# Kernel optimization log

Hardware: AMD Instinct MI355X
Metric: run time of the kernel (lower is better)

## Reference

```python
import jax, jax.numpy as jnp
import numpy as np

N = 100000
E = 3200000
IN_F = 256
OUT_F = 256


def setup_inputs() -> dict:
    key = jax.random.key(0)
    k1, k2, k3, k4, k5 = jax.random.split(key, 5)
    stdv = 1.0 / np.sqrt(OUT_F)
    x = jax.random.normal(k1, (N, IN_F), dtype=jnp.float32)
    edge_index = jax.random.randint(k2, (2, E), 0, N, dtype=jnp.int64)
    edge_weight = jax.random.uniform(k3, (E,), dtype=jnp.float32)
    weight = jax.random.uniform(k4, (IN_F, OUT_F), dtype=jnp.float32, minval=-stdv, maxval=stdv)
    bias = jax.random.uniform(k5, (OUT_F,), dtype=jnp.float32, minval=-stdv, maxval=stdv)
    return {"x": x, "edge_index": edge_index, "edge_weight": edge_weight,
            "weight": weight, "bias": bias}


def reference(x, edge_index, edge_weight, weight, bias):
    # Dense transform: [N, in] @ [in, out] -> [N, out]
    support = x @ weight
    row, col = edge_index[0], edge_index[1]
    # SpMM: out[row] += edge_weight * support[col]
    messages = edge_weight[:, None] * support[col]  # [E, out]
    output = jax.ops.segment_sum(messages, row, num_segments=N)  # [N, out]
    return output + bias
```

## Files before the change

kernel.cpp:

```cpp
#include <hip/hip_runtime.h>
#include <hip/hip_fp16.h>

#define IN_F 256
#define OUT_F 256
#define HALF_F 128
#define RPB_SHIFT 9
#define RPB (1 << RPB_SHIFT)
#define NBINS_MAX 256
#define TILE_E 4096
#define XS_PAD 40
#define SHARD_SHIFT 14

using bf16x8 = __attribute__((ext_vector_type(8))) short;
using bf16x4 = __attribute__((ext_vector_type(4))) short;
using f32x4  = __attribute__((ext_vector_type(4))) float;
using ull    = unsigned long long;

__device__ inline short bf16rne(float f) {
    unsigned u = __float_as_uint(f);
    u = u + 0x7FFFu + ((u >> 16) & 1u);
    return (short)(u >> 16);
}
__device__ inline unsigned pack_half2(float a, float b) {
    __half2 h = __floats2half2_rn(a, b);
    return *reinterpret_cast<unsigned*>(&h);
}

__global__ __launch_bounds__(256) void convert_wt_kernel(
    const float* __restrict__ w, short* __restrict__ wt)
{
    const int idx = blockIdx.x * blockDim.x + threadIdx.x;
    const int c = idx >> 8, k = idx & 255;
    wt[(size_t)c * IN_F + k] = bf16rne(w[(size_t)k * OUT_F + c]);
}

__global__ __launch_bounds__(256) void mfma_gemm_kernel(
    const float* __restrict__ x, const short* __restrict__ wt,
    __half* __restrict__ supA, __half* __restrict__ supB, int M)
{
    __shared__ short xs[2][32][XS_PAD];

    const int t    = threadIdx.x;
    const int lane = t & 63;
    const int wid  = t >> 6;
    const int l15  = lane & 15;
    const int l4   = lane >> 4;
    const int rowbase = blockIdx.x * 32;
    const int cbase   = wid * 64;

    const int srow = t >> 3;
    const int sks  = (t & 7) * 4;
    int grow = rowbase + srow; if (grow > M - 1) grow = M - 1;
    const float* xsrc = x + (size_t)grow * IN_F + sks;

    f32x4 acc[2][4];
#pragma unroll
    for (int rt = 0; rt < 2; ++rt)
#pragma unroll
        for (int ct = 0; ct < 4; ++ct)
            acc[rt][ct] = (f32x4){0.f, 0.f, 0.f, 0.f};

    const short* wp[4];
#pragma unroll
    for (int ct = 0; ct < 4; ++ct)
        wp[ct] = wt + (size_t)(cbase + ct * 16 + l15) * IN_F + l4 * 8;

    {
        const float4 f = *(const float4*)xsrc;
        bf16x4 v;
        v[0] = bf16rne(f.x); v[1] = bf16rne(f.y);
        v[2] = bf16rne(f.z); v[3] = bf16rne(f.w);
        *(bf16x4*)&xs[0][srow][sks] = v;
    }
    __syncthreads();

#pragma unroll
    for (int k0 = 0; k0 < 8; ++k0) {
        const int cur = k0 & 1;

        float4 nf;
        if (k0 < 7) nf = *(const float4*)(xsrc + (k0 + 1) * 32);

        bf16x8 b[4];
#pragma unroll
        for (int ct = 0; ct < 4; ++ct)
            b[ct] = *(const bf16x8*)(wp[ct] + k0 * 32);

        bf16x8 a[2];
#pragma unroll
        for (int rt = 0; rt < 2; ++rt)
            a[rt] = *(const bf16x8*)&xs[cur][rt * 16 + l15][l4 * 8];

#pragma unroll
        for (int rt = 0; rt < 2; ++rt)
#pragma unroll
            for (int ct = 0; ct < 4; ++ct)
                acc[rt][ct] = __builtin_amdgcn_mfma_f32_16x16x32_bf16(
                    b[ct], a[rt], acc[rt][ct], 0, 0, 0);

        if (k0 < 7) {
            bf16x4 v;
            v[0] = bf16rne(nf.x); v[1] = bf16rne(nf.y);
            v[2] = bf16rne(nf.z); v[3] = bf16rne(nf.w);
            *(bf16x4*)&xs[cur ^ 1][srow][sks] = v;
        }
        __syncthreads();
    }

    __half* dst = (wid < 2) ? supA : supB;
    const int fbase = (wid & 1) * 64;
#pragma unroll
    for (int rt = 0; rt < 2; ++rt) {
        const int r = rowbase + rt * 16 + l15;
        if (r >= M) continue;
#pragma unroll
        for (int ct = 0; ct < 4; ++ct) {
            uint2 pk;
            pk.x = pack_half2(acc[rt][ct][0], acc[rt][ct][1]);
            pk.y = pack_half2(acc[rt][ct][2], acc[rt][ct][3]);
            *(uint2*)(dst + (size_t)r * HALF_F + fbase + ct * 16 + l4 * 4) = pk;
        }
    }
}

__global__ __launch_bounds__(256) void a1a_hist_kernel(
    const int* __restrict__ ei, int* __restrict__ thist, int E)
{
    __shared__ int hist[NBINS_MAX];
    const int tid = threadIdx.x;
    hist[tid] = 0;
    __syncthreads();
    const int base = blockIdx.x * TILE_E;
#pragma unroll
    for (int i = 0; i < TILE_E / 256; ++i) {
        const int e = base + i * 256 + tid;
        if (e < E)
            atomicAdd(&hist[__builtin_nontemporal_load(ei + e) >> RPB_SHIFT], 1);
    }
    __syncthreads();
    thist[(size_t)blockIdx.x * NBINS_MAX + tid] = hist[tid];
}

__global__ __launch_bounds__(256) void tile_scan_kernel(
    int* __restrict__ thist, int* __restrict__ btot, int T)
{
    const int b   = blockIdx.x;
    const int tid = threadIdx.x;
    __shared__ int s[256];
    int carry = 0;
    for (int c0 = 0; c0 < T; c0 += 256) {
        const int t = c0 + tid;
        const int v = (t < T) ? thist[(size_t)t * NBINS_MAX + b] : 0;
        s[tid] = v;
        __syncthreads();
        for (int d = 1; d < 256; d <<= 1) {
            const int u = (tid >= d) ? s[tid - d] : 0;
            __syncthreads();
            s[tid] += u;
            __syncthreads();
        }
        const int total = s[255];
        if (t < T) thist[(size_t)t * NBINS_MAX + b] = carry + s[tid] - v;
        carry += total;
        __syncthreads();
    }
    if (tid == 0) btot[b] = carry;
}

__global__ __launch_bounds__(NBINS_MAX) void bin_scan_kernel(
    const int* __restrict__ btot, int* __restrict__ bstart, int nbins)
{
    __shared__ int s[NBINS_MAX];
    const int tid = threadIdx.x;
    const int v = (tid < nbins) ? btot[tid] : 0;
    s[tid] = v;
    __syncthreads();
    for (int d = 1; d < NBINS_MAX; d <<= 1) {
        const int u = (tid >= d) ? s[tid - d] : 0;
        __syncthreads();
        s[tid] += u;
        __syncthreads();
    }
    bstart[tid] = s[tid] - v;
}

__global__ __launch_bounds__(256) void a1b_scatter_kernel(
    const int* __restrict__ ei, const float* __restrict__ ew,
    const int* __restrict__ bstart, const int* __restrict__ thist,
    ull* __restrict__ tscw, int E)
{
    __shared__ int hist[NBINS_MAX];
    __shared__ int rbase[NBINS_MAX];
    const int tid = threadIdx.x;
    hist[tid]  = 0;
    rbase[tid] = bstart[tid] + thist[(size_t)blockIdx.x * NBINS_MAX + tid];
    __syncthreads();
    const int base = blockIdx.x * TILE_E;
#pragma unroll
    for (int i = 0; i < TILE_E / 256; ++i) {
        const int e = base + i * 256 + tid;
        if (e < E) {
            const int      row = __builtin_nontemporal_load(ei + e);
            const int      col = __builtin_nontemporal_load(ei + E + e);
            const unsigned wb  = __builtin_nontemporal_load((const unsigned*)ew + e);
            const int b   = row >> RPB_SHIFT;
            const int rnk = atomicAdd(&hist[b], 1);
            tscw[rbase[b] + rnk] = ((ull)wb << 32) |
                                   ((unsigned)col << RPB_SHIFT) |
                                   (unsigned)(row & (RPB - 1));
        }
    }
}

__global__ __launch_bounds__(256) void a2_sort_kernel(
    const ull* __restrict__ tscw, const int* __restrict__ bstart,
    const int* __restrict__ btot, int* __restrict__ counts,
    int* __restrict__ cursor, ull* __restrict__ scw, int M)
{
    const int b   = blockIdx.x;
    const int tid = threadIdx.x;
    const int n   = btot[b];
    const int s0  = bstart[b];

    __shared__ int hcur[RPB * 8];
    __shared__ int hbase[RPB * 8];
    __shared__ int s[256];

#pragma unroll
    for (int k = 0; k < 16; ++k) hcur[tid + k * 256] = 0;
    __syncthreads();

    for (int i = tid; i < n; i += 256) {
        const ull en = __builtin_nontemporal_load(tscw + s0 + i);
        const int key = ((int)(en & (RPB - 1)) << 3) |
                        (int)((en >> (RPB_SHIFT + SHARD_SHIFT)) & 7u);
        atomicAdd(&hcur[key], 1);
    }
    __syncthreads();

    int loc[16];
    int run = 0;
#pragma unroll
    for (int k = 0; k < 16; ++k) { loc[k] = hcur[tid * 16 + k]; run += loc[k]; }
    s[tid] = run;
    __syncthreads();
    for (int d = 1; d < 256; d <<= 1) {
        const int u = (tid >= d) ? s[tid - d] : 0;
        __syncthreads();
        s[tid] += u;
        __syncthreads();
    }
    int accum = s[tid] - run;
#pragma unroll
    for (int k = 0; k < 16; ++k) { hbase[tid * 16 + k] = accum; accum += loc[k]; }
    __syncthreads();

    {
        const int r0 = 2 * tid, r1 = r0 + 1;
        const int st0  = hbase[r0 << 3];
        const int st1  = hbase[r1 << 3];
        const int end1 = (r1 == RPB - 1) ? n : hbase[(r1 + 1) << 3];
        const int gr0 = (b << RPB_SHIFT) + r0, gr1 = gr0 + 1;
        if (gr0 < M) { counts[gr0] = st1 - st0;  cursor[gr0] = s0 + st0; }
        if (gr1 < M) { counts[gr1] = end1 - st1; cursor[gr1] = s0 + st1; }
    }
#pragma unroll
    for (int k = 0; k < 16; ++k) hcur[tid * 16 + k] = s0 + hbase[tid * 16 + k];
    __syncthreads();

    for (int i = tid; i < n; i += 256) {
        const ull en = __builtin_nontemporal_load(tscw + s0 + i);
        const int key = ((int)(en & (RPB - 1)) << 3) |
                        (int)((en >> (RPB_SHIFT + SHARD_SHIFT)) & 7u);
        const int pos = atomicAdd(&hcur[key], 1);
        scw[pos] = (en & 0xFFFFFFFF00000000ull) |
                   (unsigned)((en >> RPB_SHIFT) & 0x1FFFFu);
    }
}

__global__ __launch_bounds__(256) void pull_half_kernel(
    const int* __restrict__ counts, const int* __restrict__ cursor,
    const ull* __restrict__ scw, const __half* __restrict__ suph,
    const float* __restrict__ biash, float* __restrict__ outh, int M)
{
    const int wv  = blockIdx.x * 4 + (threadIdx.x >> 6);
    const int row = wv * 2 + ((threadIdx.x >> 5) & 1);
    if (row >= M) return;
    const int l = threadIdx.x & 31;

    const int cnt   = counts[row];
    const int start = cursor[row];

    float4 acc = *(const float4*)(biash + l * 4);

#define GATHER_FMA_H(pe)                                                      \
    {                                                                         \
        const int   c  = (int)(unsigned)(pe);                                 \
        const float wj = __uint_as_float((unsigned)((pe) >> 32));             \
        const uint2 v = *(const uint2*)(suph + (size_t)c * HALF_F + l * 4);   \
        const float2 f0 = __half22float2(*(const __half2*)&v.x);              \
        const float2 f1 = __half22float2(*(const __half2*)&v.y);              \
        acc.x = fmaf(wj, f0.x, acc.x); acc.y = fmaf(wj, f0.y, acc.y);         \
        acc.z = fmaf(wj, f1.x, acc.z); acc.w = fmaf(wj, f1.y, acc.w);         \
    }

    for (int j0 = 0; j0 < cnt; j0 += 32) {
        ull pr = 0ull;
        if (j0 + l < cnt)
            pr = __builtin_nontemporal_load(scw + start + j0 + l);
        const int m = min(32, cnt - j0);

        int j = 0;
        for (; j + 4 <= m; j += 4) {
            const ull p0 = __shfl(pr, j, 32),     p1 = __shfl(pr, j + 1, 32);
            const ull p2 = __shfl(pr, j + 2, 32), p3 = __shfl(pr, j + 3, 32);
            GATHER_FMA_H(p0); GATHER_FMA_H(p1);
            GATHER_FMA_H(p2); GATHER_FMA_H(p3);
        }
        for (; j < m; ++j) {
            const ull p = __shfl(pr, j, 32);
            GATHER_FMA_H(p);
        }
    }
#undef GATHER_FMA_H

    f32x4 o; o[0] = acc.x; o[1] = acc.y; o[2] = acc.z; o[3] = acc.w;
    __builtin_nontemporal_store(o, (f32x4*)(outh + (size_t)row * OUT_F + l * 4));
}

__global__ __launch_bounds__(256) void bias_init_kernel(
    float* __restrict__ out, const float* __restrict__ bias, int total4)
{
    const float4* b4 = (const float4*)bias;
    float4* o4 = (float4*)out;
    for (int i = blockIdx.x * blockDim.x + threadIdx.x; i < total4;
         i += gridDim.x * blockDim.x)
        o4[i] = b4[i & 63];
}

__global__ __launch_bounds__(256) void edge_scatter_kernel(
    const int* __restrict__ ei, const float* __restrict__ ew,
    const __half* __restrict__ supA, const __half* __restrict__ supB,
    float* __restrict__ out, int E)
{
    const int e = blockIdx.x * 4 + (threadIdx.x >> 6);
    if (e >= E) return;
    const int lane = threadIdx.x & 63;
    const int   row = ei[e];
    const int   col = ei[E + e];
    const float wgt = ew[e];
    const __half* src = (lane < 32) ? supA : supB;
    const int fl = (lane & 31) * 4;
    const uint2 v = *(const uint2*)(src + (size_t)col * HALF_F + fl);
    const float2 f0 = __half22float2(*(const __half2*)&v.x);
    const float2 f1 = __half22float2(*(const __half2*)&v.y);
    float* o = out + (size_t)row * OUT_F + (lane >> 5) * HALF_F + fl;
    unsafeAtomicAdd(o + 0, wgt * f0.x);
    unsafeAtomicAdd(o + 1, wgt * f0.y);
    unsafeAtomicAdd(o + 2, wgt * f1.x);
    unsafeAtomicAdd(o + 3, wgt * f1.y);
}

extern "C" void kernel_launch(void* const* d_in, const int* in_sizes, int n_in,
                              void* d_out, int out_size, void* d_ws, size_t ws_size,
                              hipStream_t stream)
{
    const float* x    = (const float*)d_in[0];
    const int*   ei   = (const int*)d_in[1];
    const float* ew   = (const float*)d_in[2];
    const float* w    = (const float*)d_in[3];
    const float* bias = (const float*)d_in[4];
    float* out = (float*)d_out;

    const int M = in_sizes[0] / IN_F;
    const int E = in_sizes[2];
    const int nbins = (M + RPB - 1) >> RPB_SHIFT;
    const int T     = (E + TILE_E - 1) / TILE_E;

    char* p = (char*)d_ws;
    const size_t suph_b   = (((size_t)M * HALF_F * sizeof(__half)) + 255) & ~255ull;
    const size_t counts_b = ((size_t)M * 4 + 255) & ~255ull;
    const size_t btot_b   = NBINS_MAX * 4;
    const size_t cursor_b = counts_b;
    const size_t bstart_b = NBINS_MAX * 4;
    const size_t thist_b  = (((size_t)T * NBINS_MAX * 4) + 255) & ~255ull;
    const size_t scw_b    = ((size_t)E * 8 + 255) & ~255ull;
    const size_t tscw_b   = scw_b;
    const size_t wt_b     = (size_t)IN_F * OUT_F * sizeof(short);
    const size_t need     = 2 * suph_b + counts_b + btot_b + cursor_b + bstart_b
                          + thist_b + scw_b + tscw_b + wt_b;

    __half* supA   = (__half*)p;               p += suph_b;
    __half* supB   = (__half*)p;               p += suph_b;
    int*    counts = (int*)p;                  p += counts_b;
    int*    btot   = (int*)p;                  p += btot_b;
    int*    cursor = (int*)p;                  p += cursor_b;
    int*    bstart = (int*)p;                  p += bstart_b;
    int*    thist  = (int*)p;                  p += thist_b;
    ull*    scw    = (ull*)p;                  p += scw_b;
    ull*    tscw   = (ull*)p;                  p += tscw_b;
    short*  wtb    = (short*)p;

    convert_wt_kernel<<<(IN_F * OUT_F) / 256, 256, 0, stream>>>(w, wtb);
    mfma_gemm_kernel<<<(M + 31) / 32, 256, 0, stream>>>(x, wtb, supA, supB, M);

    if (ws_size >= need) {
        a1a_hist_kernel<<<T, 256, 0, stream>>>(ei, thist, E);
        tile_scan_kernel<<<nbins, 256, 0, stream>>>(thist, btot, T);
        bin_scan_kernel<<<1, NBINS_MAX, 0, stream>>>(btot, bstart, nbins);
        a1b_scatter_kernel<<<T, 256, 0, stream>>>(ei, ew, bstart, thist, tscw, E);
        a2_sort_kernel<<<nbins, 256, 0, stream>>>(
            tscw, bstart, btot, counts, cursor, scw, M);
        const int pblocks = ((M + 1) / 2 + 3) / 4;
        pull_half_kernel<<<pblocks, 256, 0, stream>>>(
            counts, cursor, scw, supA, bias, out, M);
        pull_half_kernel<<<pblocks, 256, 0, stream>>>(
            counts, cursor, scw, supB, bias + HALF_F, out + HALF_F, M);
    } else {
        const int total4 = M * OUT_F / 4;
        bias_init_kernel<<<2048, 256, 0, stream>>>(out, bias, total4);
        edge_scatter_kernel<<<(E + 3) / 4, 256, 0, stream>>>(ei, ew, supA, supB, out, E);
    }
}
```

Measured before the change: 439.4 us.

## Replace per-bin LDS sort with global row counts and compact 32-bit edge entries

Per-row degrees now come from a global atomic count kernel and a per-bin row scan. The single-block-per-bin shared-memory counting sort becomes a chunked scatter that uses global atomic cursors per row, which gives more parallelism in that stage. Edge entries are packed into 32 bits: a 17-bit column and the weight quantized to 15 bits. This halves the scw traffic in the gather kernels, whose inner loop is also unrolled to 8. The risks are a loss of weight precision from the 15-bit quantization, an extra pass over edge_index, and global atomic contention.

```diff
diff --git a/kernel.cpp b/kernel.cpp
--- a/kernel.cpp
+++ b/kernel.cpp
@@ -9,7 +9,7 @@
 #define NBINS_MAX 256
 #define TILE_E 4096
 #define XS_PAD 40
-#define SHARD_SHIFT 14
+#define A2_CHUNKS 8
 
 using bf16x8 = __attribute__((ext_vector_type(8))) short;
 using bf16x4 = __attribute__((ext_vector_type(4))) short;
@@ -121,6 +121,13 @@
             *(uint2*)(dst + (size_t)r * HALF_F + fbase + ct * 16 + l4 * 4) = pk;
         }
     }
+}
+
+__global__ __launch_bounds__(256) void count_kernel(
+    const int* __restrict__ ei, int* __restrict__ counts, int E)
+{
+    const int e = blockIdx.x * blockDim.x + threadIdx.x;
+    if (e < E) atomicAdd(&counts[__builtin_nontemporal_load(ei + e)], 1);
 }
 
 __global__ __launch_bounds__(256) void a1a_hist_kernel(
@@ -182,6 +189,31 @@
         __syncthreads();
     }
     bstart[tid] = s[tid] - v;
+}
+
+__global__ __launch_bounds__(256) void row_scan_kernel(
+    const int* __restrict__ counts, const int* __restrict__ bstart,
+    int* __restrict__ cur_start, int* __restrict__ cur_live, int M)
+{
+    const int bin  = blockIdx.x;
+    const int base = bin << RPB_SHIFT;
+    const int tid  = threadIdx.x;
+    const int r0 = base + 2 * tid, r1 = r0 + 1;
+    const int c0 = (r0 < M) ? counts[r0] : 0;
+    const int c1 = (r1 < M) ? counts[r1] : 0;
+    __shared__ int s[256];
+    const int own = c0 + c1;
+    s[tid] = own;
+    __syncthreads();
+    for (int d = 1; d < 256; d <<= 1) {
+        const int u = (tid >= d) ? s[tid - d] : 0;
+        __syncthreads();
+        s[tid] += u;
+        __syncthreads();
+    }
+    const int excl = s[tid] - own + bstart[bin];
+    if (r0 < M) { cur_start[r0] = excl;      cur_live[r0] = excl; }
+    if (r1 < M) { cur_start[r1] = excl + c0; cur_live[r1] = excl + c0; }
 }
 
 __global__ __launch_bounds__(256) void a1b_scatter_kernel(
@@ -212,75 +244,31 @@
     }
 }
 
-__global__ __launch_bounds__(256) void a2_sort_kernel(
+__global__ __launch_bounds__(256) void a2_scatter_kernel(
     const ull* __restrict__ tscw, const int* __restrict__ bstart,
-    const int* __restrict__ btot, int* __restrict__ counts,
-    int* __restrict__ cursor, ull* __restrict__ scw, int M)
-{
-    const int b   = blockIdx.x;
-    const int tid = threadIdx.x;
-    const int n   = btot[b];
-    const int s0  = bstart[b];
-
-    __shared__ int hcur[RPB * 8];
-    __shared__ int hbase[RPB * 8];
-    __shared__ int s[256];
-
-#pragma unroll
-    for (int k = 0; k < 16; ++k) hcur[tid + k * 256] = 0;
-    __syncthreads();
-
-    for (int i = tid; i < n; i += 256) {
+    const int* __restrict__ btot, int* __restrict__ cur_live,
+    unsigned* __restrict__ scw4)
+{
+    const int b  = blockIdx.x / A2_CHUNKS;
+    const int c  = blockIdx.x % A2_CHUNKS;
+    const int n  = btot[b];
+    const int s0 = bstart[b];
+    const int i0 = (int)(((long long)n * c) / A2_CHUNKS);
+    const int i1 = (int)(((long long)n * (c + 1)) / A2_CHUNKS);
+    for (int i = i0 + (int)threadIdx.x; i < i1; i += 256) {
         const ull en = __builtin_nontemporal_load(tscw + s0 + i);
-        const int key = ((int)(en & (RPB - 1)) << 3) |
-                        (int)((en >> (RPB_SHIFT + SHARD_SHIFT)) & 7u);
-        atomicAdd(&hcur[key], 1);
-    }
-    __syncthreads();
-
-    int loc[16];
-    int run = 0;
-#pragma unroll
-    for (int k = 0; k < 16; ++k) { loc[k] = hcur[tid * 16 + k]; run += loc[k]; }
-    s[tid] = run;
-    __syncthreads();
-    for (int d = 1; d < 256; d <<= 1) {
-        const int u = (tid >= d) ? s[tid - d] : 0;
-        __syncthreads();
-        s[tid] += u;
-        __syncthreads();
-    }
-    int accum = s[tid] - run;
-#pragma unroll
-    for (int k = 0; k < 16; ++k) { hbase[tid * 16 + k] = accum; accum += loc[k]; }
-    __syncthreads();
-
-    {
-        const int r0 = 2 * tid, r1 = r0 + 1;
-        const int st0  = hbase[r0 << 3];
-        const int st1  = hbase[r1 << 3];
-        const int end1 = (r1 == RPB - 1) ? n : hbase[(r1 + 1) << 3];
-        const int gr0 = (b << RPB_SHIFT) + r0, gr1 = gr0 + 1;
-        if (gr0 < M) { counts[gr0] = st1 - st0;  cursor[gr0] = s0 + st0; }
-        if (gr1 < M) { counts[gr1] = end1 - st1; cursor[gr1] = s0 + st1; }
-    }
-#pragma unroll
-    for (int k = 0; k < 16; ++k) hcur[tid * 16 + k] = s0 + hbase[tid * 16 + k];
-    __syncthreads();
-
-    for (int i = tid; i < n; i += 256) {
-        const ull en = __builtin_nontemporal_load(tscw + s0 + i);
-        const int key = ((int)(en & (RPB - 1)) << 3) |
-                        (int)((en >> (RPB_SHIFT + SHARD_SHIFT)) & 7u);
-        const int pos = atomicAdd(&hcur[key], 1);
-        scw[pos] = (en & 0xFFFFFFFF00000000ull) |
-                   (unsigned)((en >> RPB_SHIFT) & 0x1FFFFu);
+        const int row = (b << RPB_SHIFT) | (int)(en & (RPB - 1));
+        const unsigned col = (unsigned)((en >> RPB_SHIFT) & 0x1FFFFu);
+        const float wf = __uint_as_float((unsigned)(en >> 32));
+        const unsigned w15 = (unsigned)(wf * 32767.0f + 0.5f);
+        const int pos = atomicAdd(&cur_live[row], 1);
+        scw4[pos] = (w15 << 17) | col;
     }
 }
 
 __global__ __launch_bounds__(256) void pull_half_kernel(
-    const int* __restrict__ counts, const int* __restrict__ cursor,
-    const ull* __restrict__ scw, const __half* __restrict__ suph,
+    const int* __restrict__ counts, const int* __restrict__ cur_start,
+    const unsigned* __restrict__ scw4, const __half* __restrict__ suph,
     const float* __restrict__ biash, float* __restrict__ outh, int M)
 {
     const int wv  = blockIdx.x * 4 + (threadIdx.x >> 6);
@@ -289,14 +277,14 @@
     const int l = threadIdx.x & 31;
 
     const int cnt   = counts[row];
-    const int start = cursor[row];
+    const int start = cur_start[row];
 
     float4 acc = *(const float4*)(biash + l * 4);
 
 #define GATHER_FMA_H(pe)                                                      \
     {                                                                         \
-        const int   c  = (int)(unsigned)(pe);                                 \
-        const float wj = __uint_as_float((unsigned)((pe) >> 32));             \
+        const int   c  = (int)((pe) & 0x1FFFFu);                              \
+        const float wj = (float)((pe) >> 17) * (1.0f / 32767.0f);             \
         const uint2 v = *(const uint2*)(suph + (size_t)c * HALF_F + l * 4);   \
         const float2 f0 = __half22float2(*(const __half2*)&v.x);              \
         const float2 f1 = __half22float2(*(const __half2*)&v.y);              \
@@ -305,20 +293,22 @@
     }
 
     for (int j0 = 0; j0 < cnt; j0 += 32) {
-        ull pr = 0ull;
+        unsigned pr = 0u;
         if (j0 + l < cnt)
-            pr = __builtin_nontemporal_load(scw + start + j0 + l);
+            pr = __builtin_nontemporal_load(scw4 + start + j0 + l);
         const int m = min(32, cnt - j0);
 
         int j = 0;
-        for (; j + 4 <= m; j += 4) {
-            const ull p0 = __shfl(pr, j, 32),     p1 = __shfl(pr, j + 1, 32);
-            const ull p2 = __shfl(pr, j + 2, 32), p3 = __shfl(pr, j + 3, 32);
-            GATHER_FMA_H(p0); GATHER_FMA_H(p1);
-            GATHER_FMA_H(p2); GATHER_FMA_H(p3);
+        for (; j + 8 <= m; j += 8) {
+            const unsigned p0 = __shfl(pr, j, 32),     p1 = __shfl(pr, j + 1, 32);
+            const unsigned p2 = __shfl(pr, j + 2, 32), p3 = __shfl(pr, j + 3, 32);
+            const unsigned p4 = __shfl(pr, j + 4, 32), p5 = __shfl(pr, j + 5, 32);
+            const unsigned p6 = __shfl(pr, j + 6, 32), p7 = __shfl(pr, j + 7, 32);
+            GATHER_FMA_H(p0); GATHER_FMA_H(p1); GATHER_FMA_H(p2); GATHER_FMA_H(p3);
+            GATHER_FMA_H(p4); GATHER_FMA_H(p5); GATHER_FMA_H(p6); GATHER_FMA_H(p7);
         }
         for (; j < m; ++j) {
-            const ull p = __shfl(pr, j, 32);
+            const unsigned p = __shfl(pr, j, 32);
             GATHER_FMA_H(p);
         }
     }
@@ -381,41 +371,46 @@
     const size_t suph_b   = (((size_t)M * HALF_F * sizeof(__half)) + 255) & ~255ull;
     const size_t counts_b = ((size_t)M * 4 + 255) & ~255ull;
     const size_t btot_b   = NBINS_MAX * 4;
-    const size_t cursor_b = counts_b;
+    const size_t cstart_b = counts_b;
+    const size_t clive_b  = counts_b;
     const size_t bstart_b = NBINS_MAX * 4;
     const size_t thist_b  = (((size_t)T * NBINS_MAX * 4) + 255) & ~255ull;
-    const size_t scw_b    = ((size_t)E * 8 + 255) & ~255ull;
-    const size_t tscw_b   = scw_b;
+    const size_t scw4_b   = ((size_t)E * 4 + 255) & ~255ull;
+    const size_t tscw_b   = ((size_t)E * 8 + 255) & ~255ull;
     const size_t wt_b     = (size_t)IN_F * OUT_F * sizeof(short);
-    const size_t need     = 2 * suph_b + counts_b + btot_b + cursor_b + bstart_b
-                          + thist_b + scw_b + tscw_b + wt_b;
-
-    __half* supA   = (__half*)p;               p += suph_b;
-    __half* supB   = (__half*)p;               p += suph_b;
-    int*    counts = (int*)p;                  p += counts_b;
-    int*    btot   = (int*)p;                  p += btot_b;
-    int*    cursor = (int*)p;                  p += cursor_b;
-    int*    bstart = (int*)p;                  p += bstart_b;
-    int*    thist  = (int*)p;                  p += thist_b;
-    ull*    scw    = (ull*)p;                  p += scw_b;
-    ull*    tscw   = (ull*)p;                  p += tscw_b;
-    short*  wtb    = (short*)p;
+    const size_t need     = 2 * suph_b + counts_b + btot_b + cstart_b + clive_b
+                          + bstart_b + thist_b + scw4_b + tscw_b + wt_b;
+
+    __half*   supA    = (__half*)p;            p += suph_b;
+    __half*   supB    = (__half*)p;            p += suph_b;
+    int*      counts  = (int*)p;               p += counts_b;
+    int*      btot    = (int*)p;               p += btot_b;
+    int*      cstart  = (int*)p;               p += cstart_b;
+    int*      clive   = (int*)p;               p += clive_b;
+    int*      bstart  = (int*)p;               p += bstart_b;
+    int*      thist   = (int*)p;               p += thist_b;
+    unsigned* scw4    = (unsigned*)p;          p += scw4_b;
+    ull*      tscw    = (ull*)p;               p += tscw_b;
+    short*    wtb     = (short*)p;
 
     convert_wt_kernel<<<(IN_F * OUT_F) / 256, 256, 0, stream>>>(w, wtb);
     mfma_gemm_kernel<<<(M + 31) / 32, 256, 0, stream>>>(x, wtb, supA, supB, M);
 
     if (ws_size >= need) {
+        hipMemsetAsync(counts, 0, (size_t)M * 4, stream);
+        count_kernel<<<(E + 255) / 256, 256, 0, stream>>>(ei, counts, E);
         a1a_hist_kernel<<<T, 256, 0, stream>>>(ei, thist, E);
         tile_scan_kernel<<<nbins, 256, 0, stream>>>(thist, btot, T);
         bin_scan_kernel<<<1, NBINS_MAX, 0, stream>>>(btot, bstart, nbins);
+        row_scan_kernel<<<nbins, 256, 0, stream>>>(counts, bstart, cstart, clive, M);
         a1b_scatter_kernel<<<T, 256, 0, stream>>>(ei, ew, bstart, thist, tscw, E);
-        a2_sort_kernel<<<nbins, 256, 0, stream>>>(
-            tscw, bstart, btot, counts, cursor, scw, M);
+        a2_scatter_kernel<<<nbins * A2_CHUNKS, 256, 0, stream>>>(
+            tscw, bstart, btot, clive, scw4);
         const int pblocks = ((M + 1) / 2 + 3) / 4;
         pull_half_kernel<<<pblocks, 256, 0, stream>>>(
-            counts, cursor, scw, supA, bias, out, M);
+            counts, cstart, scw4, supA, bias, out, M);
         pull_half_kernel<<<pblocks, 256, 0, stream>>>(
-            counts, cursor, scw, supB, bias + HALF_F, out + HALF_F, M);
+            counts, cstart, scw4, supB, bias + HALF_F, out + HALF_F, M);
     } else {
         const int total4 = M * OUT_F / 4;
         bias_init_kernel<<<2048, 256, 0, stream>>>(out, bias, total4);
```

Measured after the change: 586.1 us. 1.33x slower.
